# Kernel tuning notes

Hardware: AMD Instinct MI355X
Metric: run time of the kernel (lower is better)

Reference implementation:

```python
import jax, jax.numpy as jnp
import numpy as np

N_NODES = 100000
N_EDGES = 1200000
D_IN = 64
D_HID = 64


def setup_inputs() -> dict:
    key = jax.random.key(0)
    k1, k2, k3, k4 = jax.random.split(key, 4)
    x = jax.random.normal(k1, (N_NODES, D_IN), dtype=jnp.float32)
    edge_index = jax.random.randint(k2, (2, N_EDGES), 0, N_NODES, dtype=jnp.int32)
    edge_attr = jax.random.uniform(k3, (N_EDGES,), dtype=jnp.float32)
    W = jax.random.normal(k4, (D_HID, D_IN), dtype=jnp.float32) / np.sqrt(D_IN)
    b = jnp.zeros((D_HID,), dtype=jnp.float32)
    return {"x": x, "edge_index": edge_index, "edge_attr": edge_attr, "W": W, "b": b}


def _gcn_conv(x, edge_index, edge_weight, W, b):
    # PyG GCNConv: add self-loops (weight 1), symmetric normalization,
    # linear transform, scatter-add aggregation at target (col), bias.
    n = x.shape[0]
    loop = jnp.arange(n, dtype=edge_index.dtype)
    row = jnp.concatenate([edge_index[0], loop])  # source
    col = jnp.concatenate([edge_index[1], loop])  # target
    ew = jnp.concatenate([edge_weight, jnp.ones((n,), edge_weight.dtype)])
    deg = jax.ops.segment_sum(ew, col, num_segments=n)  # [N]
    dis = jnp.where(deg > 0, jax.lax.rsqrt(deg), 0.0)
    norm = dis[row] * ew * dis[col]                     # [E+N]
    h = x @ W.T                                          # [N, D_HID]
    msg = norm[:, None] * h[row]                         # [E+N, D_HID]
    out = jax.ops.segment_sum(msg, col, num_segments=n)  # [N, D_HID]
    return out + b


def reference(x, edge_index, edge_attr, W, b):
    # layer_num=2 -> single GCNConv; dropout is identity in eval mode.
    h = _gcn_conv(x, edge_index, edge_attr, W, b)
    return jax.nn.relu(h)
```

## Files before the change

### kernel.cpp

```cpp
#include <hip/hip_runtime.h>

#define N_NODES 100000
#define N_EDGES 1200000
#define D 64
#define KP 68
#define TN 64
#define CAP 48
#define Q15 32767.0f
#define INVQ15 (1.0f / 32767.0f)
#define BW 512
#define BSH 9
#define NBKT ((N_NODES + BW - 1) / BW)
#define CAPB 8192
#define N4 (N_EDGES / 4)
#define NB_COARSE ((N4 + 511) / 512)
#define NB_GEMM ((N_NODES + TN - 1) / TN)

__device__ __forceinline__ unsigned short f2bf(float f) {
    unsigned u = __float_as_uint(f);
    return (unsigned short)((u + 0x7FFFu + ((u >> 16) & 1u)) >> 16);
}
__device__ __forceinline__ float bf2f(unsigned short h) {
    return __uint_as_float((unsigned)h << 16);
}

__global__ __launch_bounds__(256) void k_pre(const int4* __restrict__ row4,
                                             const int4* __restrict__ col4,
                                             const float4* __restrict__ ew4,
                                             int* __restrict__ gcur,
                                             int2* __restrict__ coarse,
                                             const float* __restrict__ x,
                                             const float* __restrict__ W,
                                             unsigned short* __restrict__ hb,
                                             int n4, int n_nodes) {
    __shared__ int lcnt[NBKT];
    __shared__ int lbase[NBKT];
    __shared__ float wt[D * KP];
    int t = threadIdx.x;

    if (blockIdx.x < NB_COARSE) {
        for (int i = t; i < NBKT; i += 256) lcnt[i] = 0;
        __syncthreads();

        int bkt[8]; int slot[8]; int2 rec[8];
        #pragma unroll
        for (int k = 0; k < 8; k++) bkt[k] = -1;

        #pragma unroll
        for (int r = 0; r < 2; r++) {
            int q = blockIdx.x * 512 + r * 256 + t;
            if (q < n4) {
                int4 rr = row4[q]; int4 cc = col4[q]; float4 ww = ew4[q];
                int j = r * 4;
                int c;
                c = cc.x; bkt[j+0] = c >> BSH;
                rec[j+0] = make_int2(rr.x, ((c & (BW-1)) << 15) | (int)(ww.x * Q15 + 0.5f));
                slot[j+0] = atomicAdd(&lcnt[bkt[j+0]], 1);
                c = cc.y; bkt[j+1] = c >> BSH;
                rec[j+1] = make_int2(rr.y, ((c & (BW-1)) << 15) | (int)(ww.y * Q15 + 0.5f));
                slot[j+1] = atomicAdd(&lcnt[bkt[j+1]], 1);
                c = cc.z; bkt[j+2] = c >> BSH;
                rec[j+2] = make_int2(rr.z, ((c & (BW-1)) << 15) | (int)(ww.z * Q15 + 0.5f));
                slot[j+2] = atomicAdd(&lcnt[bkt[j+2]], 1);
                c = cc.w; bkt[j+3] = c >> BSH;
                rec[j+3] = make_int2(rr.w, ((c & (BW-1)) << 15) | (int)(ww.w * Q15 + 0.5f));
                slot[j+3] = atomicAdd(&lcnt[bkt[j+3]], 1);
            }
        }
        __syncthreads();
        for (int i = t; i < NBKT; i += 256) {
            int c = lcnt[i];
            lbase[i] = c ? atomicAdd(&gcur[i], c) : 0;
        }
        __syncthreads();
        #pragma unroll
        for (int k = 0; k < 8; k++) {
            if (bkt[k] >= 0) {
                int pos = lbase[bkt[k]] + slot[k];
                if (pos < CAPB) coarse[(size_t)bkt[k] * CAPB + pos] = rec[k];
            }
        }
    } else {
        int base = (blockIdx.x - NB_COARSE) * TN;
        #pragma unroll
        for (int c = 0; c < 16; c++) {
            int idx = t + c * 256;
            wt[(idx & 63) * KP + (idx >> 6)] = W[idx];
        }
        __syncthreads();

        int tx = t & 15, ty = t >> 4;
        int f0 = tx * 4, n0 = base + ty * 4;
        const float* xr0 = x + (size_t)min(n0 + 0, n_nodes - 1) * D;
        const float* xr1 = x + (size_t)min(n0 + 1, n_nodes - 1) * D;
        const float* xr2 = x + (size_t)min(n0 + 2, n_nodes - 1) * D;
        const float* xr3 = x + (size_t)min(n0 + 3, n_nodes - 1) * D;

        float acc[4][4] = {};
        #pragma unroll 4
        for (int k = 0; k < D; k += 4) {
            float a[4][4], wv[4][4];
            *(float4*)a[0] = *(const float4*)&xr0[k];
            *(float4*)a[1] = *(const float4*)&xr1[k];
            *(float4*)a[2] = *(const float4*)&xr2[k];
            *(float4*)a[3] = *(const float4*)&xr3[k];
            #pragma unroll
            for (int kk = 0; kk < 4; kk++)
                *(float4*)wv[kk] = *(const float4*)&wt[(k + kk) * KP + f0];
            #pragma unroll
            for (int kk = 0; kk < 4; kk++)
                #pragma unroll
                for (int j = 0; j < 4; j++)
                    #pragma unroll
                    for (int ff = 0; ff < 4; ff++)
                        acc[j][ff] = fmaf(a[j][kk], wv[kk][ff], acc[j][ff]);
        }
        #pragma unroll
        for (int j = 0; j < 4; j++) {
            int n = n0 + j;
            if (n < n_nodes) {
                unsigned short h0 = f2bf(acc[j][0]);
                unsigned short h1 = f2bf(acc[j][1]);
                unsigned short h2 = f2bf(acc[j][2]);
                unsigned short h3 = f2bf(acc[j][3]);
                uint2 pk;
                pk.x = (unsigned)h0 | ((unsigned)h1 << 16);
                pk.y = (unsigned)h2 | ((unsigned)h3 << 16);
                *(uint2*)&hb[(size_t)n * D + f0] = pk;
            }
        }
    }
}

__global__ __launch_bounds__(1024) void k_bin(const int* __restrict__ gcur,
                                              const int2* __restrict__ coarse,
                                              int* __restrict__ cnt,
                                              float* __restrict__ dis,
                                              unsigned int* __restrict__ em, int n_nodes) {
    __shared__ int   cur512[BW];
    __shared__ float d512[BW];
    int b = blockIdx.x, t = threadIdx.x;
    int total = min(gcur[b], CAPB);
    int nbase = b * BW;
    int bw = min(BW, n_nodes - nbase);
    for (int i = t; i < BW; i += 1024) { cur512[i] = 0; d512[i] = 0.f; }
    __syncthreads();
    const int2* src = &coarse[(size_t)b * CAPB];
    for (int i = t; i < total; i += 1024) {
        int2 r = src[i];
        int cl = (r.y >> 15) & (BW - 1);
        float w = (float)(r.y & 0x7FFF) * INVQ15;
        int s = atomicAdd(&cur512[cl], 1);
        atomicAdd(&d512[cl], w);
        if (s < CAP)
            em[(size_t)(nbase + cl) * CAP + s] = ((unsigned)r.x << 15) | (unsigned)(r.y & 0x7FFF);
    }
    __syncthreads();
    for (int i = t; i < bw; i += 1024) {
        cnt[nbase + i] = cur512[i];
        dis[nbase + i] = rsqrtf(1.0f + d512[i]);
    }
}

__global__ __launch_bounds__(256) void k_agg_cap(const int* __restrict__ cnt,
                                                 const unsigned int* __restrict__ em,
                                                 const unsigned short* __restrict__ hb,
                                                 const float* __restrict__ dis,
                                                 const float* __restrict__ b,
                                                 float* __restrict__ out, int n_nodes) {
    int w = threadIdx.x >> 6, l = threadIdx.x & 63;
    int n0 = blockIdx.x * 8 + w * 2;
    int n1 = n0 + 1;
    int c0 = min(cnt[n0], CAP);
    int c1 = min(cnt[n1], CAP);
    unsigned r0 = em[(size_t)n0 * CAP + min(l, max(c0 - 1, 0))];
    unsigned r1 = em[(size_t)n1 * CAP + min(l, max(c1 - 1, 0))];
    int   off0 = (int)(r0 >> 15) * D;
    int   off1 = (int)(r1 >> 15) * D;
    float wg0 = (float)(r0 & 0x7FFFu) * INVQ15 * dis[r0 >> 15];
    float wg1 = (float)(r1 & 0x7FFFu) * INVQ15 * dis[r1 >> 15];
    float ds0 = dis[n0], ds1 = dis[n1];
    float acc0 = ds0 * bf2f(hb[(size_t)n0 * D + l]);
    float acc1 = ds1 * bf2f(hb[(size_t)n1 * D + l]);

    int i0 = 0, i1 = 0;
    while (i0 + 4 <= c0 && i1 + 4 <= c1) {
        int   oa0 = __shfl(off0, i0 + 0), oa1 = __shfl(off0, i0 + 1);
        int   oa2 = __shfl(off0, i0 + 2), oa3 = __shfl(off0, i0 + 3);
        int   ob0 = __shfl(off1, i1 + 0), ob1 = __shfl(off1, i1 + 1);
        int   ob2 = __shfl(off1, i1 + 2), ob3 = __shfl(off1, i1 + 3);
        float va0 = __shfl(wg0, i0 + 0), va1 = __shfl(wg0, i0 + 1);
        float va2 = __shfl(wg0, i0 + 2), va3 = __shfl(wg0, i0 + 3);
        float vb0 = __shfl(wg1, i1 + 0), vb1 = __shfl(wg1, i1 + 1);
        float vb2 = __shfl(wg1, i1 + 2), vb3 = __shfl(wg1, i1 + 3);
        float ha0 = bf2f(hb[oa0 + l]);
        float ha1 = bf2f(hb[oa1 + l]);
        float ha2 = bf2f(hb[oa2 + l]);
        float ha3 = bf2f(hb[oa3 + l]);
        float hb0 = bf2f(hb[ob0 + l]);
        float hb1 = bf2f(hb[ob1 + l]);
        float hb2 = bf2f(hb[ob2 + l]);
        float hb3 = bf2f(hb[ob3 + l]);
        acc0 = fmaf(va0, ha0, acc0);
        acc0 = fmaf(va1, ha1, acc0);
        acc0 = fmaf(va2, ha2, acc0);
        acc0 = fmaf(va3, ha3, acc0);
        acc1 = fmaf(vb0, hb0, acc1);
        acc1 = fmaf(vb1, hb1, acc1);
        acc1 = fmaf(vb2, hb2, acc1);
        acc1 = fmaf(vb3, hb3, acc1);
        i0 += 4; i1 += 4;
    }
    for (; i0 + 4 <= c0; i0 += 4) {
        int   oa0 = __shfl(off0, i0 + 0), oa1 = __shfl(off0, i0 + 1);
        int   oa2 = __shfl(off0, i0 + 2), oa3 = __shfl(off0, i0 + 3);
        float va0 = __shfl(wg0, i0 + 0), va1 = __shfl(wg0, i0 + 1);
        float va2 = __shfl(wg0, i0 + 2), va3 = __shfl(wg0, i0 + 3);
        float ha0 = bf2f(hb[oa0 + l]);
        float ha1 = bf2f(hb[oa1 + l]);
        float ha2 = bf2f(hb[oa2 + l]);
        float ha3 = bf2f(hb[oa3 + l]);
        acc0 = fmaf(va0, ha0, acc0);
        acc0 = fmaf(va1, ha1, acc0);
        acc0 = fmaf(va2, ha2, acc0);
        acc0 = fmaf(va3, ha3, acc0);
    }
    for (; i0 < c0; i0++) {
        int   o = __shfl(off0, i0);
        float v = __shfl(wg0, i0);
        acc0 = fmaf(v, bf2f(hb[o + l]), acc0);
    }
    for (; i1 + 4 <= c1; i1 += 4) {
        int   ob0 = __shfl(off1, i1 + 0), ob1 = __shfl(off1, i1 + 1);
        int   ob2 = __shfl(off1, i1 + 2), ob3 = __shfl(off1, i1 + 3);
        float vb0 = __shfl(wg1, i1 + 0), vb1 = __shfl(wg1, i1 + 1);
        float vb2 = __shfl(wg1, i1 + 2), vb3 = __shfl(wg1, i1 + 3);
        float hb0 = bf2f(hb[ob0 + l]);
        float hb1 = bf2f(hb[ob1 + l]);
        float hb2 = bf2f(hb[ob2 + l]);
        float hb3 = bf2f(hb[ob3 + l]);
        acc1 = fmaf(vb0, hb0, acc1);
        acc1 = fmaf(vb1, hb1, acc1);
        acc1 = fmaf(vb2, hb2, acc1);
        acc1 = fmaf(vb3, hb3, acc1);
    }
    for (; i1 < c1; i1++) {
        int   o = __shfl(off1, i1);
        float v = __shfl(wg1, i1);
        acc1 = fmaf(v, bf2f(hb[o + l]), acc1);
    }

    float bl = b[l];
    float v0 = fmaf(ds0, acc0, bl);
    float v1 = fmaf(ds1, acc1, bl);
    out[(size_t)n0 * D + l] = v0 > 0.f ? v0 : 0.f;
    out[(size_t)n1 * D + l] = v1 > 0.f ? v1 : 0.f;
}

extern "C" void kernel_launch(void* const* d_in, const int* in_sizes, int n_in,
                              void* d_out, int out_size, void* d_ws, size_t ws_size,
                              hipStream_t stream) {
    const float* x   = (const float*)d_in[0];
    const int*   ei  = (const int*)d_in[1];
    const float* ew  = (const float*)d_in[2];
    const float* W   = (const float*)d_in[3];
    const float* b   = (const float*)d_in[4];
    float* out = (float*)d_out;

    const int* row = ei;
    const int* col = ei + N_EDGES;

    char* p = (char*)d_ws;
    auto carve = [&](size_t bytes) { char* q = p; p += (bytes + 255) & ~(size_t)255; return q; };
    float*          dis    = (float*)carve(N_NODES * sizeof(float));
    unsigned short* hb     = (unsigned short*)carve((size_t)N_NODES * D * sizeof(unsigned short));
    int*            cnt    = (int*)  carve(N_NODES * sizeof(int));
    unsigned int*   em     = (unsigned int*)carve((size_t)N_NODES * CAP * sizeof(unsigned int));
    int*            gcur   = (int*)  carve(NBKT * sizeof(int));
    int2*           coarse = (int2*) carve((size_t)NBKT * CAPB * sizeof(int2));

    hipMemsetAsync(gcur, 0, NBKT * sizeof(int), stream);

    k_pre<<<NB_COARSE + NB_GEMM, 256, 0, stream>>>(
        (const int4*)row, (const int4*)col, (const float4*)ew, gcur, coarse,
        x, W, hb, N4, N_NODES);
    k_bin<<<NBKT, 1024, 0, stream>>>(gcur, coarse, cnt, dis, em, N_NODES);
    k_agg_cap<<<N_NODES / 8, 256, 0, stream>>>(cnt, em, hb, dis, b, out, N_NODES);
}
```

Baseline: 170.2 us.

## Store per-node edge lists as compact CSR via in-block prefix scan and LDS sort

The bin kernel now counts per-node edges, runs a shared-memory prefix scan, scatters packed edges into an LDS-sorted buffer and writes them out contiguously. It replaces the fixed 48-slot per-node padded edge array with a compact CSR-style layout, and each node gets a packed base/count word. This cuts scattered writes and the padded footprint of the edge array, which should improve locality for the aggregation loads. In exchange, the bin kernel makes a second pass over the coarse data and uses 32KB of LDS plus a scan. The count is capped at 63 instead of 48.

```diff
diff --git a/kernel.cpp b/kernel.cpp
--- a/kernel.cpp
+++ b/kernel.cpp
@@ -5,7 +5,6 @@
 #define D 64
 #define KP 68
 #define TN 64
-#define CAP 48
 #define Q15 32767.0f
 #define INVQ15 (1.0f / 32767.0f)
 #define BW 512
@@ -134,35 +133,61 @@
 
 __global__ __launch_bounds__(1024) void k_bin(const int* __restrict__ gcur,
                                               const int2* __restrict__ coarse,
-                                              int* __restrict__ cnt,
+                                              unsigned int* __restrict__ pb,
                                               float* __restrict__ dis,
                                               unsigned int* __restrict__ em, int n_nodes) {
-    __shared__ int   cur512[BW];
-    __shared__ float d512[BW];
+    __shared__ int   lcnt[BW];
+    __shared__ int   lofs[BW];
+    __shared__ int   lcur[BW];
+    __shared__ float dw[BW];
+    __shared__ unsigned int sorted[CAPB];
     int b = blockIdx.x, t = threadIdx.x;
     int total = min(gcur[b], CAPB);
     int nbase = b * BW;
     int bw = min(BW, n_nodes - nbase);
-    for (int i = t; i < BW; i += 1024) { cur512[i] = 0; d512[i] = 0.f; }
+    if (t < BW) { lcnt[t] = 0; lcur[t] = 0; dw[t] = 0.f; }
     __syncthreads();
     const int2* src = &coarse[(size_t)b * CAPB];
+
     for (int i = t; i < total; i += 1024) {
         int2 r = src[i];
         int cl = (r.y >> 15) & (BW - 1);
-        float w = (float)(r.y & 0x7FFF) * INVQ15;
-        int s = atomicAdd(&cur512[cl], 1);
-        atomicAdd(&d512[cl], w);
-        if (s < CAP)
-            em[(size_t)(nbase + cl) * CAP + s] = ((unsigned)r.x << 15) | (unsigned)(r.y & 0x7FFF);
+        atomicAdd(&lcnt[cl], 1);
+        atomicAdd(&dw[cl], (float)(r.y & 0x7FFF) * INVQ15);
     }
     __syncthreads();
-    for (int i = t; i < bw; i += 1024) {
-        cnt[nbase + i] = cur512[i];
-        dis[nbase + i] = rsqrtf(1.0f + d512[i]);
-    }
-}
-
-__global__ __launch_bounds__(256) void k_agg_cap(const int* __restrict__ cnt,
+
+    int ocnt = (t < BW) ? lcnt[t] : 0;
+    for (int d = 1; d < BW; d <<= 1) {
+        int v = 0;
+        if (t < BW && t >= d) v = lcnt[t - d];
+        __syncthreads();
+        if (t < BW) lcnt[t] += v;
+        __syncthreads();
+    }
+    if (t < BW) {
+        int ofs = lcnt[t] - ocnt;
+        lofs[t] = ofs;
+        if (t < bw) {
+            pb[nbase + t] = ((unsigned)(b * CAPB + ofs) << 6) | (unsigned)min(ocnt, 63);
+            dis[nbase + t] = rsqrtf(1.0f + dw[t]);
+        }
+    }
+    __syncthreads();
+
+    for (int i = t; i < total; i += 1024) {
+        int2 r = src[i];
+        int cl = (r.y >> 15) & (BW - 1);
+        int s = atomicAdd(&lcur[cl], 1);
+        sorted[lofs[cl] + s] = ((unsigned)r.x << 15) | (unsigned)(r.y & 0x7FFF);
+    }
+    __syncthreads();
+
+    for (int i = t; i < total; i += 1024)
+        em[(size_t)b * CAPB + i] = sorted[i];
+}
+
+__global__ __launch_bounds__(256) void k_agg_cap(const unsigned int* __restrict__ pb,
                                                  const unsigned int* __restrict__ em,
                                                  const unsigned short* __restrict__ hb,
                                                  const float* __restrict__ dis,
@@ -171,10 +196,11 @@
     int w = threadIdx.x >> 6, l = threadIdx.x & 63;
     int n0 = blockIdx.x * 8 + w * 2;
     int n1 = n0 + 1;
-    int c0 = min(cnt[n0], CAP);
-    int c1 = min(cnt[n1], CAP);
-    unsigned r0 = em[(size_t)n0 * CAP + min(l, max(c0 - 1, 0))];
-    unsigned r1 = em[(size_t)n1 * CAP + min(l, max(c1 - 1, 0))];
+    unsigned p0 = pb[n0], p1 = pb[n1];
+    int c0 = (int)(p0 & 63u), c1 = (int)(p1 & 63u);
+    unsigned base0 = p0 >> 6, base1 = p1 >> 6;
+    unsigned r0 = em[base0 + min(l, max(c0 - 1, 0))];
+    unsigned r1 = em[base1 + min(l, max(c1 - 1, 0))];
     int   off0 = (int)(r0 >> 15) * D;
     int   off1 = (int)(r1 >> 15) * D;
     float wg0 = (float)(r0 & 0x7FFFu) * INVQ15 * dis[r0 >> 15];
@@ -274,8 +300,8 @@
     auto carve = [&](size_t bytes) { char* q = p; p += (bytes + 255) & ~(size_t)255; return q; };
     float*          dis    = (float*)carve(N_NODES * sizeof(float));
     unsigned short* hb     = (unsigned short*)carve((size_t)N_NODES * D * sizeof(unsigned short));
-    int*            cnt    = (int*)  carve(N_NODES * sizeof(int));
-    unsigned int*   em     = (unsigned int*)carve((size_t)N_NODES * CAP * sizeof(unsigned int));
+    unsigned int*   pb     = (unsigned int*)carve(N_NODES * sizeof(unsigned int));
+    unsigned int*   em     = (unsigned int*)carve(((size_t)NBKT * CAPB + 64) * sizeof(unsigned int));
     int*            gcur   = (int*)  carve(NBKT * sizeof(int));
     int2*           coarse = (int2*) carve((size_t)NBKT * CAPB * sizeof(int2));
 
@@ -284,6 +310,6 @@
     k_pre<<<NB_COARSE + NB_GEMM, 256, 0, stream>>>(
         (const int4*)row, (const int4*)col, (const float4*)ew, gcur, coarse,
         x, W, hb, N4, N_NODES);
-    k_bin<<<NBKT, 1024, 0, stream>>>(gcur, coarse, cnt, dis, em, N_NODES);
-    k_agg_cap<<<N_NODES / 8, 256, 0, stream>>>(cnt, em, hb, dis, b, out, N_NODES);
-}
+    k_bin<<<NBKT, 1024, 0, stream>>>(gcur, coarse, pb, dis, em, N_NODES);
+    k_agg_cap<<<N_NODES / 8, 256, 0, stream>>>(pb, em, hb, dis, b, out, N_NODES);
+}
```

After: 168.9 us. No clear change (-0.8%).
